# Kernel tuning notes

Measured on AMD Instinct MI355X. Metric: run time of the kernel, lower is better.

## Reference

```python
import jax, jax.numpy as jnp
import numpy as np

N_Q = 4       # n_qubits
PATCH = 3
PAD = 1       # patch_size // 2


def _u3(theta, phi, lam):
    # U3 gate matrix (2x2 complex)
    c = jnp.cos(theta / 2)
    s = jnp.sin(theta / 2)
    row0 = jnp.stack([c + 0j, -jnp.exp(1j * lam) * s])
    row1 = jnp.stack([jnp.exp(1j * phi) * s, jnp.exp(1j * (phi + lam)) * c])
    return jnp.stack([row0, row1]).astype(jnp.complex64)


def _apply_1q(state, U, wire):
    # state: (N,2,2,2,2) complex; U: (2,2) shared or (N,2,2) batched
    s = jnp.moveaxis(state, 1 + wire, -1)
    shp = s.shape
    s = s.reshape(s.shape[0], -1, 2)
    if U.ndim == 2:
        out = jnp.einsum('ij,nrj->nri', U, s)
    else:
        out = jnp.einsum('nij,nrj->nri', U, s)
    return jnp.moveaxis(out.reshape(shp), -1, 1 + wire)


def _apply_2q(state, U4, cw, tw):
    # U4: (4,4) on (control, target) subspace ordered |c t>
    s = jnp.moveaxis(state, (1 + cw, 1 + tw), (-2, -1))
    shp = s.shape
    s = s.reshape(s.shape[0], -1, 4)
    out = jnp.einsum('ij,nrj->nri', U4, s)
    return jnp.moveaxis(out.reshape(shp), (-2, -1), (1 + cw, 1 + tw))


def setup_inputs() -> dict:
    key = jax.random.key(0)
    ks = jax.random.split(key, 8)
    B, C, H, W = 16, 64, 64, 64
    out_ch = 128
    d_in = C * PATCH * PATCH  # 576
    x = jax.random.normal(ks[0], (B, C, H, W), dtype=jnp.float32)
    fc1_w = jax.random.normal(ks[1], (N_Q, d_in), dtype=jnp.float32) * (1.0 / np.sqrt(d_in))
    fc1_b = jax.random.normal(ks[2], (N_Q,), dtype=jnp.float32) * 0.01
    u3_params = jax.random.normal(ks[3], (N_Q, 3), dtype=jnp.float32)
    cu3_params = jax.random.normal(ks[4], (N_Q, 3), dtype=jnp.float32)
    fc_w = jax.random.normal(ks[5], (out_ch, N_Q), dtype=jnp.float32) * 0.5
    fc_b = jax.random.normal(ks[6], (out_ch,), dtype=jnp.float32) * 0.01
    return {"x": x, "fc1_w": fc1_w, "fc1_b": fc1_b, "u3_params": u3_params,
            "cu3_params": cu3_params, "fc_w": fc_w, "fc_b": fc_b}


def reference(x, fc1_w, fc1_b, u3_params, cu3_params, fc_w, fc_b):
    B, C, H, W = x.shape
    xp = jnp.pad(x, ((0, 0), (0, 0), (PAD, PAD), (PAD, PAD)))
    Hout, Wout = H, W  # stride 1, same padding
    # im2col: feature order (C, di, dj) matches torch patch.reshape(B,-1)
    cols = jnp.stack([xp[:, :, di:di + Hout, dj:dj + Wout]
                      for di in range(PATCH) for dj in range(PATCH)], axis=2)  # (B,C,9,H,W)
    patches = cols.transpose(0, 3, 4, 1, 2).reshape(B, Hout * Wout, C * PATCH * PATCH)
    ang = patches @ fc1_w.T + fc1_b  # (B, P, 4) rotation angles
    Np = B * Hout * Wout
    ang = ang.reshape(Np, N_Q)
    # initial state |0000> for every (batch, patch)
    state = jnp.zeros((Np, 2 ** N_Q), jnp.complex64).at[:, 0].set(1.0)
    state = state.reshape((Np,) + (2,) * N_Q)
    # RY encoding (per-element angles)
    for w in range(N_Q):
        th = ang[:, w] / 2
        c, s = jnp.cos(th), jnp.sin(th)
        Ury = jnp.stack([jnp.stack([c, -s], -1), jnp.stack([s, c], -1)], -2).astype(jnp.complex64)
        state = _apply_1q(state, Ury, w)
    # trainable U3 on every wire
    for w in range(N_Q):
        state = _apply_1q(state, _u3(u3_params[w, 0], u3_params[w, 1], u3_params[w, 2]), w)
    # circular CU3 ring (0,1),(1,2),(2,3),(3,0)
    for w in range(N_Q):
        U = _u3(cu3_params[w, 0], cu3_params[w, 1], cu3_params[w, 2])
        U4 = jnp.eye(4, dtype=jnp.complex64).at[2:, 2:].set(U)
        state = _apply_2q(state, U4, w, (w + 1) % N_Q)
    # <Z> on each wire
    probs = state.real ** 2 + state.imag ** 2  # (Np,2,2,2,2)
    zv = jnp.array([1.0, -1.0], jnp.float32)
    expz = jnp.stack(
        [(probs * zv.reshape((1,) + (1,) * w + (2,) + (1,) * (N_Q - 1 - w))).sum(axis=(1, 2, 3, 4))
         for w in range(N_Q)], axis=1)  # (Np,4)
    out = expz.reshape(B, Hout * Wout, N_Q) @ fc_w.T + fc_b  # (B,P,out_ch)
    out_ch = fc_w.shape[0]
    # faithful to original: view(B, out_ch, side_h, side_w) on contiguous (P,out_ch)
    return out.reshape(B, out_ch, Hout, Wout)
```

## Files before the change

kernel.cpp:

```cpp
#include <hip/hip_runtime.h>
#include <hip/hip_bf16.h>
#include <math.h>

typedef unsigned short u16;
typedef unsigned int   u32;
typedef unsigned long long u64;

#define WS_W2    0
#define WS_B4    2304
#define WS_FCW   2308
#define WS_FCB   2820
#define WS_GATES 2948
#define WS_FLAG  3012
#define WS_PART  4096

__device__ inline float bfbits2f(u32 lo16) {
    u32 u = lo16 << 16;
    return __builtin_bit_cast(float, u);
}
__device__ inline float bchi(u32 w) {
    return __builtin_bit_cast(float, w & 0xffff0000u);
}
__device__ inline float bclo(u32 w) {
    return __builtin_bit_cast(float, w << 16);
}
__device__ inline u16 f2bf(float f) {
    u32 u = __builtin_bit_cast(u32, f);
    u = u + 0x7fffu + ((u >> 16) & 1u);
    return (u16)(u >> 16);
}
__device__ inline float ld_param(const void* p, int i, int isbf16) {
    return isbf16 ? bfbits2f(((const u16*)p)[i]) : ((const float*)p)[i];
}

__global__ __launch_bounds__(256) void k0_prep(
        const void* __restrict__ x,
        const void* __restrict__ fc1_w, const void* __restrict__ fc1_b,
        const void* __restrict__ u3p,   const void* __restrict__ cu3p,
        const void* __restrict__ fc_w,  const void* __restrict__ fc_b,
        float* __restrict__ ws) {
    __shared__ int sflag;
    int t = threadIdx.x;
    if (t == 0) {
        const u32* xw = (const u32*)x;
        int cnt = 0;
        for (int i = 0; i < 64; ++i) {
            u32 e = (xw[i] >> 7) & 0xFFu;
            if (e >= 110 && e <= 130) ++cnt;
        }
        sflag = (cnt >= 32) ? 1 : 0;
        ws[WS_FLAG] = (float)sflag;
    }
    __syncthreads();
    const int bf = sflag;
    u32* wpk = (u32*)ws + WS_W2;
    for (int idx = t; idx < 1152; idx += 256) {
        int c = idx / 18;
        int rem = idx - c * 18;
        int r = rem / 6;
        int p = rem - r * 6;
        int i0 = 2 * p, i1 = 2 * p + 1;
        int q0 = i0 / 3, d0 = i0 - 3 * q0;
        int q1 = i1 / 3, d1 = i1 - 3 * q1;
        u32 lo = f2bf(ld_param(fc1_w, q0 * 576 + c * 9 + r * 3 + d0, bf));
        u32 hi = f2bf(ld_param(fc1_w, q1 * 576 + c * 9 + r * 3 + d1, bf));
        wpk[idx] = lo | (hi << 16);
    }
    if (t < 4)   ws[WS_B4 + t] = ld_param(fc1_b, t, bf);
    for (int idx = t; idx < 512; idx += 256) ws[WS_FCW + idx] = ld_param(fc_w, idx, bf);
    if (t < 128) ws[WS_FCB + t] = ld_param(fc_b, t, bf);
    if (t < 8) {
        int w = t & 3;
        const void* p = (t < 4) ? u3p : cu3p;
        float th = ld_param(p, w * 3 + 0, bf);
        float ph = ld_param(p, w * 3 + 1, bf);
        float la = ld_param(p, w * 3 + 2, bf);
        float c = cosf(0.5f * th), s = sinf(0.5f * th);
        float cl = cosf(la), sl = sinf(la);
        float cp = cosf(ph), sp = sinf(ph);
        float cpl = cp * cl - sp * sl, spl = sp * cl + cp * sl;
        float* m = ws + WS_GATES + t * 8;
        m[0] = c;        m[1] = 0.f;
        m[2] = -cl * s;  m[3] = -sl * s;
        m[4] = cp * s;   m[5] = sp * s;
        m[6] = cpl * c;  m[7] = spl * c;
    }
}

__global__ __launch_bounds__(256) void kA_conv(
        const void* __restrict__ x, const float* __restrict__ ws,
        float4* __restrict__ part) {
    __shared__ u32 tile[24 * 34];
    __shared__ float4 red4[256];
    const int t = threadIdx.x;
    const int bid = blockIdx.x;
    const int cg  = bid & 7;
    const int row = (bid >> 3) & 63;
    const int b   = bid >> 9;
    const int bf = (ws[WS_FLAG] != 0.0f) ? 1 : 0;
    const int c0 = cg * 8;
    const int tc = t >> 6;

    const int cs = __builtin_amdgcn_readfirstlane(c0 + tc * 2);
    const u32* wpk = (const u32*)ws + WS_W2 + cs * 18;
    u32 w36[36];
#pragma unroll
    for (int i = 0; i < 36; ++i) w36[i] = wpk[i];

    const u32*    xu = (const u32*)x;
    const float2* xf = (const float2*)x;
    const int xbase = b * 131072;

    {
        const int jj = t & 31;
        const int g8 = t >> 5;
#pragma unroll
        for (int i = 0; i < 3; ++i) {
            int rowcl = g8 + i * 8;
            int r = rowcl >> 3, cl = rowcl & 7;
            int gr = row - 1 + r;
            u32 pk = 0;
            if (gr >= 0 && gr < 64) {
                int idx = xbase + (c0 + cl) * 2048 + gr * 32 + jj;
                if (bf) pk = xu[idx];
                else { float2 v = xf[idx];
                       pk = (u32)f2bf(v.x) | ((u32)f2bf(v.y) << 16); }
            }
            tile[rowcl * 34 + 1 + jj] = pk;
        }
        if (t < 48) { int rc = t >> 1; tile[rc * 34 + ((t & 1) ? 33 : 0)] = 0u; }
    }
    __syncthreads();

    const int j = t & 63;
    const int pj = (j + 1) >> 1;
    const int sh = (1 - (j & 1)) * 16;
    float ang0 = 0.f, ang1 = 0.f, ang2 = 0.f, ang3 = 0.f;
#pragma unroll
    for (int cc = 0; cc < 2; ++cc) {
        const int cl = tc * 2 + cc;
#pragma unroll
        for (int r = 0; r < 3; ++r) {
            const u32* rp = tile + (r * 8 + cl) * 34 + pj;
            u32 lo = rp[0], hi = rp[1];
            u64 v = (((u64)hi << 32) | lo) >> sh;
            u32 vlo = (u32)v, vhi = (u32)(v >> 32);
            float e0 = bclo(vlo);
            float e1 = bchi(vlo);
            float e2 = bclo(vhi);
            const int wb = cc * 18 + r * 6;
            u32 u0 = w36[wb], u1 = w36[wb + 1], u2 = w36[wb + 2];
            u32 u3 = w36[wb + 3], u4 = w36[wb + 4], u5 = w36[wb + 5];
            ang0 += e0 * bclo(u0) + e1 * bchi(u0) + e2 * bclo(u1);
            ang1 += e0 * bchi(u1) + e1 * bclo(u2) + e2 * bchi(u2);
            ang2 += e0 * bclo(u3) + e1 * bchi(u3) + e2 * bclo(u4);
            ang3 += e0 * bchi(u4) + e1 * bclo(u5) + e2 * bchi(u5);
        }
    }

    red4[tc * 64 + j] = make_float4(ang0, ang1, ang2, ang3);
    __syncthreads();
    if (t < 64) {
        float4 a0 = red4[t], a1 = red4[64 + t], a2 = red4[128 + t], a3 = red4[192 + t];
        float4 s = make_float4(a0.x + a1.x + a2.x + a3.x,
                               a0.y + a1.y + a2.y + a3.y,
                               a0.z + a1.z + a2.z + a3.z,
                               a0.w + a1.w + a2.w + a3.w);
        part[cg * 65536 + b * 4096 + row * 64 + t] = s;
    }
}

__global__ __launch_bounds__(256) void kB_circuit_fc(
        const float* __restrict__ ws, const float4* __restrict__ part,
        void* __restrict__ out) {
    __shared__ float4 smEz[64];
    const int t = threadIdx.x;
    const int bp0 = blockIdx.x * 64;
    const int bf = (ws[WS_FLAG] != 0.0f) ? 1 : 0;

    if (t < 64) {
        const int bp = bp0 + t;
        float ax = 0.f, ay = 0.f, az = 0.f, aw = 0.f;
#pragma unroll
        for (int g = 0; g < 8; ++g) {
            float4 a = part[g * 65536 + bp];
            ax += a.x; ay += a.y; az += a.z; aw += a.w;
        }
        float angf[4];
        angf[0] = ws[WS_B4 + 0] + ax;
        angf[1] = ws[WS_B4 + 1] + ay;
        angf[2] = ws[WS_B4 + 2] + az;
        angf[3] = ws[WS_B4 + 3] + aw;

        const float* G = ws + WS_GATES;
        float vr[4][2], vi[4][2];
#pragma unroll
        for (int w = 0; w < 4; ++w) {
            float sa, ca;
            __sincosf(0.5f * angf[w], &sa, &ca);
            const float* m = G + w * 8;
            vr[w][0] = m[0] * ca + m[2] * sa;  vi[w][0] = m[1] * ca + m[3] * sa;
            vr[w][1] = m[4] * ca + m[6] * sa;  vi[w][1] = m[5] * ca + m[7] * sa;
        }
        float t01r[4], t01i[4], t23r[4], t23i[4];
#pragma unroll
        for (int a = 0; a < 2; ++a)
#pragma unroll
            for (int bq = 0; bq < 2; ++bq) {
                t01r[a * 2 + bq] = vr[0][a] * vr[1][bq] - vi[0][a] * vi[1][bq];
                t01i[a * 2 + bq] = vr[0][a] * vi[1][bq] + vi[0][a] * vr[1][bq];
                t23r[a * 2 + bq] = vr[2][a] * vr[3][bq] - vi[2][a] * vi[3][bq];
                t23i[a * 2 + bq] = vr[2][a] * vi[3][bq] + vi[2][a] * vr[3][bq];
            }
        float ar[16], ai[16];
#pragma unroll
        for (int n = 0; n < 16; ++n) {
            int hi = n >> 2, lo = n & 3;
            ar[n] = t01r[hi] * t23r[lo] - t01i[hi] * t23i[lo];
            ai[n] = t01r[hi] * t23i[lo] + t01i[hi] * t23r[lo];
        }
#pragma unroll
        for (int w = 0; w < 4; ++w) {
            const float* m = G + 32 + w * 8;
            const int cb = 8 >> w;
            const int tb = 8 >> ((w + 1) & 3);
#pragma unroll
            for (int n = 0; n < 16; ++n) {
                if ((n & cb) != 0 && (n & tb) == 0) {
                    int n1 = n | tb;
                    float a0r = ar[n], a0i = ai[n], a1r = ar[n1], a1i = ai[n1];
                    ar[n]  = m[0] * a0r - m[1] * a0i + m[2] * a1r - m[3] * a1i;
                    ai[n]  = m[0] * a0i + m[1] * a0r + m[2] * a1i + m[3] * a1r;
                    ar[n1] = m[4] * a0r - m[5] * a0i + m[6] * a1r - m[7] * a1i;
                    ai[n1] = m[4] * a0i + m[5] * a0r + m[6] * a1i + m[7] * a1r;
                }
            }
        }
        float ez[4] = {0.f, 0.f, 0.f, 0.f};
#pragma unroll
        for (int n = 0; n < 16; ++n) {
            float pr = ar[n] * ar[n] + ai[n] * ai[n];
#pragma unroll
            for (int w = 0; w < 4; ++w)
                ez[w] += ((n >> (3 - w)) & 1) ? -pr : pr;
        }
        smEz[t] = make_float4(ez[0], ez[1], ez[2], ez[3]);
    }
    __syncthreads();

    const int og = (t & 15) * 8;
    const float4* fw4 = (const float4*)(ws + WS_FCW) + og;
    const float*  fbp = ws + WS_FCB + og;
    float4 w0 = fw4[0], w1 = fw4[1], w2 = fw4[2], w3 = fw4[3];
    float4 w4 = fw4[4], w5 = fw4[5], w6 = fw4[6], w7 = fw4[7];
    float4 bA = *(const float4*)fbp, bB = *(const float4*)(fbp + 4);
#pragma unroll
    for (int ch = 0; ch < 4; ++ch) {
        const int pl = (t >> 4) + ch * 16;
        const float4 ez = smEz[pl];
        float v0 = bA.x + ez.x*w0.x + ez.y*w0.y + ez.z*w0.z + ez.w*w0.w;
        float v1 = bA.y + ez.x*w1.x + ez.y*w1.y + ez.z*w1.z + ez.w*w1.w;
        float v2 = bA.z + ez.x*w2.x + ez.y*w2.y + ez.z*w2.z + ez.w*w2.w;
        float v3 = bA.w + ez.x*w3.x + ez.y*w3.y + ez.z*w3.z + ez.w*w3.w;
        float v4 = bB.x + ez.x*w4.x + ez.y*w4.y + ez.z*w4.z + ez.w*w4.w;
        float v5 = bB.y + ez.x*w5.x + ez.y*w5.y + ez.z*w5.z + ez.w*w5.w;
        float v6 = bB.z + ez.x*w6.x + ez.y*w6.y + ez.z*w6.z + ez.w*w6.w;
        float v7 = bB.w + ez.x*w7.x + ez.y*w7.y + ez.z*w7.z + ez.w*w7.w;
        if (bf) {
            u32 p0 = (u32)f2bf(v0) | ((u32)f2bf(v1) << 16);
            u32 p1 = (u32)f2bf(v2) | ((u32)f2bf(v3) << 16);
            u32 p2 = (u32)f2bf(v4) | ((u32)f2bf(v5) << 16);
            u32 p3 = (u32)f2bf(v6) | ((u32)f2bf(v7) << 16);
            ((uint4*)out)[blockIdx.x * 1024 + ch * 256 + t] =
                make_uint4(p0, p1, p2, p3);
        } else {
            float4* o = (float4*)out + (blockIdx.x * 2048 + ch * 512 + 2 * t);
            o[0] = make_float4(v0, v1, v2, v3);
            o[1] = make_float4(v4, v5, v6, v7);
        }
    }
}

extern "C" void kernel_launch(void* const* d_in, const int* in_sizes, int n_in,
                              void* d_out, int out_size, void* d_ws, size_t ws_size,
                              hipStream_t stream) {
    float* ws = (float*)d_ws;
    float4* part = (float4*)(ws + WS_PART);
    k0_prep<<<dim3(1), dim3(256), 0, stream>>>(d_in[0], d_in[1], d_in[2], d_in[3],
                                               d_in[4], d_in[5], d_in[6], ws);
    kA_conv<<<dim3(8192), dim3(256), 0, stream>>>(d_in[0], ws, part);
    kB_circuit_fc<<<dim3(1024), dim3(256), 0, stream>>>(ws, part, d_out);
}
```

Before: 109.3 us.

## Fuse conv projection and circuit+FC kernels into one per-row block

Merges the conv/angle kernel and the circuit+FC kernel into one kernel where each 512-thread block handles all 64 channels of one output row. The 8-way channel-group partials are reduced in shared memory instead of going through a global workspace, which removes a kernel launch and the partial-sum write and read. In exchange each block stages a much larger LDS tile (192x34 words plus reductions), which lowers occupancy, and it loads weights in a serial chunk loop.

```diff
diff --git a/kernel.cpp b/kernel.cpp
--- a/kernel.cpp
+++ b/kernel.cpp
@@ -12,7 +12,6 @@
 #define WS_FCB   2820
 #define WS_GATES 2948
 #define WS_FLAG  3012
-#define WS_PART  4096
 
 __device__ inline float bfbits2f(u32 lo16) {
     u32 u = lo16 << 16;
@@ -87,25 +86,17 @@
     }
 }
 
-__global__ __launch_bounds__(256) void kA_conv(
+__global__ __launch_bounds__(512) void kF_fused(
         const void* __restrict__ x, const float* __restrict__ ws,
-        float4* __restrict__ part) {
-    __shared__ u32 tile[24 * 34];
-    __shared__ float4 red4[256];
-    const int t = threadIdx.x;
-    const int bid = blockIdx.x;
-    const int cg  = bid & 7;
-    const int row = (bid >> 3) & 63;
-    const int b   = bid >> 9;
+        void* __restrict__ out) {
+    __shared__ u32 tile[192 * 34];
+    __shared__ float4 red4[512];
+    __shared__ float4 smEz[64];
+    const int t   = threadIdx.x;
+    const int blk = blockIdx.x;
+    const int row = blk & 63;
+    const int b   = blk >> 6;
     const int bf = (ws[WS_FLAG] != 0.0f) ? 1 : 0;
-    const int c0 = cg * 8;
-    const int tc = t >> 6;
-
-    const int cs = __builtin_amdgcn_readfirstlane(c0 + tc * 2);
-    const u32* wpk = (const u32*)ws + WS_W2 + cs * 18;
-    u32 w36[36];
-#pragma unroll
-    for (int i = 0; i < 36; ++i) w36[i] = wpk[i];
 
     const u32*    xu = (const u32*)x;
     const float2* xf = (const float2*)x;
@@ -113,77 +104,66 @@
 
     {
         const int jj = t & 31;
-        const int g8 = t >> 5;
-#pragma unroll
-        for (int i = 0; i < 3; ++i) {
-            int rowcl = g8 + i * 8;
-            int r = rowcl >> 3, cl = rowcl & 7;
+        const int g  = t >> 5;
+#pragma unroll
+        for (int i = 0; i < 12; ++i) {
+            int rowcl = g + i * 16;
+            int r = rowcl >> 6, c = rowcl & 63;
             int gr = row - 1 + r;
             u32 pk = 0;
             if (gr >= 0 && gr < 64) {
-                int idx = xbase + (c0 + cl) * 2048 + gr * 32 + jj;
+                int idx = xbase + c * 2048 + gr * 32 + jj;
                 if (bf) pk = xu[idx];
                 else { float2 v = xf[idx];
                        pk = (u32)f2bf(v.x) | ((u32)f2bf(v.y) << 16); }
             }
             tile[rowcl * 34 + 1 + jj] = pk;
         }
-        if (t < 48) { int rc = t >> 1; tile[rc * 34 + ((t & 1) ? 33 : 0)] = 0u; }
-    }
-    __syncthreads();
-
-    const int j = t & 63;
+        if (t < 384) { int rc = t >> 1; tile[rc * 34 + ((t & 1) ? 33 : 0)] = 0u; }
+    }
+    __syncthreads();
+
+    const int j  = t & 63;
+    const int tcw = t >> 6;
     const int pj = (j + 1) >> 1;
     const int sh = (1 - (j & 1)) * 16;
     float ang0 = 0.f, ang1 = 0.f, ang2 = 0.f, ang3 = 0.f;
-#pragma unroll
-    for (int cc = 0; cc < 2; ++cc) {
-        const int cl = tc * 2 + cc;
-#pragma unroll
-        for (int r = 0; r < 3; ++r) {
-            const u32* rp = tile + (r * 8 + cl) * 34 + pj;
-            u32 lo = rp[0], hi = rp[1];
-            u64 v = (((u64)hi << 32) | lo) >> sh;
-            u32 vlo = (u32)v, vhi = (u32)(v >> 32);
-            float e0 = bclo(vlo);
-            float e1 = bchi(vlo);
-            float e2 = bclo(vhi);
-            const int wb = cc * 18 + r * 6;
-            u32 u0 = w36[wb], u1 = w36[wb + 1], u2 = w36[wb + 2];
-            u32 u3 = w36[wb + 3], u4 = w36[wb + 4], u5 = w36[wb + 5];
-            ang0 += e0 * bclo(u0) + e1 * bchi(u0) + e2 * bclo(u1);
-            ang1 += e0 * bchi(u1) + e1 * bclo(u2) + e2 * bchi(u2);
-            ang2 += e0 * bclo(u3) + e1 * bchi(u3) + e2 * bclo(u4);
-            ang3 += e0 * bchi(u4) + e1 * bclo(u5) + e2 * bchi(u5);
-        }
-    }
-
-    red4[tc * 64 + j] = make_float4(ang0, ang1, ang2, ang3);
-    __syncthreads();
+#pragma unroll 1
+    for (int chunk = 0; chunk < 4; ++chunk) {
+        const int cs = __builtin_amdgcn_readfirstlane(tcw * 8 + chunk * 2);
+        const u32* wpk = (const u32*)ws + WS_W2 + cs * 18;
+        u32 w36[36];
+#pragma unroll
+        for (int i = 0; i < 36; ++i) w36[i] = wpk[i];
+#pragma unroll
+        for (int cc = 0; cc < 2; ++cc) {
+#pragma unroll
+            for (int r = 0; r < 3; ++r) {
+                const u32* rp = tile + (r * 64 + cs + cc) * 34 + pj;
+                u32 lo = rp[0], hi = rp[1];
+                u64 v = (((u64)hi << 32) | lo) >> sh;
+                u32 vlo = (u32)v, vhi = (u32)(v >> 32);
+                float e0 = bclo(vlo);
+                float e1 = bchi(vlo);
+                float e2 = bclo(vhi);
+                const int wb = cc * 18 + r * 6;
+                u32 u0 = w36[wb], u1 = w36[wb + 1], u2 = w36[wb + 2];
+                u32 u3 = w36[wb + 3], u4 = w36[wb + 4], u5 = w36[wb + 5];
+                ang0 += e0 * bclo(u0) + e1 * bchi(u0) + e2 * bclo(u1);
+                ang1 += e0 * bchi(u1) + e1 * bclo(u2) + e2 * bchi(u2);
+                ang2 += e0 * bclo(u3) + e1 * bchi(u3) + e2 * bclo(u4);
+                ang3 += e0 * bchi(u4) + e1 * bclo(u5) + e2 * bchi(u5);
+            }
+        }
+    }
+    red4[t] = make_float4(ang0, ang1, ang2, ang3);
+    __syncthreads();
+
     if (t < 64) {
-        float4 a0 = red4[t], a1 = red4[64 + t], a2 = red4[128 + t], a3 = red4[192 + t];
-        float4 s = make_float4(a0.x + a1.x + a2.x + a3.x,
-                               a0.y + a1.y + a2.y + a3.y,
-                               a0.z + a1.z + a2.z + a3.z,
-                               a0.w + a1.w + a2.w + a3.w);
-        part[cg * 65536 + b * 4096 + row * 64 + t] = s;
-    }
-}
-
-__global__ __launch_bounds__(256) void kB_circuit_fc(
-        const float* __restrict__ ws, const float4* __restrict__ part,
-        void* __restrict__ out) {
-    __shared__ float4 smEz[64];
-    const int t = threadIdx.x;
-    const int bp0 = blockIdx.x * 64;
-    const int bf = (ws[WS_FLAG] != 0.0f) ? 1 : 0;
-
-    if (t < 64) {
-        const int bp = bp0 + t;
         float ax = 0.f, ay = 0.f, az = 0.f, aw = 0.f;
 #pragma unroll
-        for (int g = 0; g < 8; ++g) {
-            float4 a = part[g * 65536 + bp];
+        for (int k = 0; k < 8; ++k) {
+            float4 a = red4[k * 64 + t];
             ax += a.x; ay += a.y; az += a.z; aw += a.w;
         }
         float angf[4];
@@ -255,8 +235,8 @@
     float4 w4 = fw4[4], w5 = fw4[5], w6 = fw4[6], w7 = fw4[7];
     float4 bA = *(const float4*)fbp, bB = *(const float4*)(fbp + 4);
 #pragma unroll
-    for (int ch = 0; ch < 4; ++ch) {
-        const int pl = (t >> 4) + ch * 16;
+    for (int ch = 0; ch < 2; ++ch) {
+        const int pl = (t >> 4) + ch * 32;
         const float4 ez = smEz[pl];
         float v0 = bA.x + ez.x*w0.x + ez.y*w0.y + ez.z*w0.z + ez.w*w0.w;
         float v1 = bA.y + ez.x*w1.x + ez.y*w1.y + ez.z*w1.z + ez.w*w1.w;
@@ -271,10 +251,10 @@
             u32 p1 = (u32)f2bf(v2) | ((u32)f2bf(v3) << 16);
             u32 p2 = (u32)f2bf(v4) | ((u32)f2bf(v5) << 16);
             u32 p3 = (u32)f2bf(v6) | ((u32)f2bf(v7) << 16);
-            ((uint4*)out)[blockIdx.x * 1024 + ch * 256 + t] =
+            ((uint4*)out)[blk * 1024 + ch * 512 + t] =
                 make_uint4(p0, p1, p2, p3);
         } else {
-            float4* o = (float4*)out + (blockIdx.x * 2048 + ch * 512 + 2 * t);
+            float4* o = (float4*)out + (blk * 2048 + ch * 1024 + 2 * t);
             o[0] = make_float4(v0, v1, v2, v3);
             o[1] = make_float4(v4, v5, v6, v7);
         }
@@ -285,9 +265,7 @@
                               void* d_out, int out_size, void* d_ws, size_t ws_size,
                               hipStream_t stream) {
     float* ws = (float*)d_ws;
-    float4* part = (float4*)(ws + WS_PART);
     k0_prep<<<dim3(1), dim3(256), 0, stream>>>(d_in[0], d_in[1], d_in[2], d_in[3],
                                                d_in[4], d_in[5], d_in[6], ws);
-    kA_conv<<<dim3(8192), dim3(256), 0, stream>>>(d_in[0], ws, part);
-    kB_circuit_fc<<<dim3(1024), dim3(256), 0, stream>>>(ws, part, d_out);
-}
+    kF_fused<<<dim3(1024), dim3(512), 0, stream>>>(d_in[0], ws, d_out);
+}
```

Result: slower. 116.3 us (+6.4%).

## Drop prep kernel; fold param prep into conv and circuit kernels, stage partials in output

Applied to the files above, without the earlier changes.

Removes the single-block prep kernel by having each block sniff the input dtype with a wavefront ballot and load or convert fc1 weights, gate matrices and FC params directly from the inputs. Partial angle sums are now staged in the output buffer, laid out per row-block so each circuit block reads only its own region before overwriting it. This saves one launch and its serialization, at the cost of redundant per-block weight conversion and trig work. The in-place reuse of the output relies on each block's read region lying inside its own write region.

```diff
diff --git a/kernel.cpp b/kernel.cpp
--- a/kernel.cpp
+++ b/kernel.cpp
@@ -5,14 +5,6 @@
 typedef unsigned short u16;
 typedef unsigned int   u32;
 typedef unsigned long long u64;
-
-#define WS_W2    0
-#define WS_B4    2304
-#define WS_FCW   2308
-#define WS_FCB   2820
-#define WS_GATES 2948
-#define WS_FLAG  3012
-#define WS_PART  4096
 
 __device__ inline float bfbits2f(u32 lo16) {
     u32 u = lo16 << 16;
@@ -33,63 +25,16 @@
     return isbf16 ? bfbits2f(((const u16*)p)[i]) : ((const float*)p)[i];
 }
 
-__global__ __launch_bounds__(256) void k0_prep(
-        const void* __restrict__ x,
-        const void* __restrict__ fc1_w, const void* __restrict__ fc1_b,
-        const void* __restrict__ u3p,   const void* __restrict__ cu3p,
-        const void* __restrict__ fc_w,  const void* __restrict__ fc_b,
-        float* __restrict__ ws) {
-    __shared__ int sflag;
-    int t = threadIdx.x;
-    if (t == 0) {
-        const u32* xw = (const u32*)x;
-        int cnt = 0;
-        for (int i = 0; i < 64; ++i) {
-            u32 e = (xw[i] >> 7) & 0xFFu;
-            if (e >= 110 && e <= 130) ++cnt;
-        }
-        sflag = (cnt >= 32) ? 1 : 0;
-        ws[WS_FLAG] = (float)sflag;
-    }
-    __syncthreads();
-    const int bf = sflag;
-    u32* wpk = (u32*)ws + WS_W2;
-    for (int idx = t; idx < 1152; idx += 256) {
-        int c = idx / 18;
-        int rem = idx - c * 18;
-        int r = rem / 6;
-        int p = rem - r * 6;
-        int i0 = 2 * p, i1 = 2 * p + 1;
-        int q0 = i0 / 3, d0 = i0 - 3 * q0;
-        int q1 = i1 / 3, d1 = i1 - 3 * q1;
-        u32 lo = f2bf(ld_param(fc1_w, q0 * 576 + c * 9 + r * 3 + d0, bf));
-        u32 hi = f2bf(ld_param(fc1_w, q1 * 576 + c * 9 + r * 3 + d1, bf));
-        wpk[idx] = lo | (hi << 16);
-    }
-    if (t < 4)   ws[WS_B4 + t] = ld_param(fc1_b, t, bf);
-    for (int idx = t; idx < 512; idx += 256) ws[WS_FCW + idx] = ld_param(fc_w, idx, bf);
-    if (t < 128) ws[WS_FCB + t] = ld_param(fc_b, t, bf);
-    if (t < 8) {
-        int w = t & 3;
-        const void* p = (t < 4) ? u3p : cu3p;
-        float th = ld_param(p, w * 3 + 0, bf);
-        float ph = ld_param(p, w * 3 + 1, bf);
-        float la = ld_param(p, w * 3 + 2, bf);
-        float c = cosf(0.5f * th), s = sinf(0.5f * th);
-        float cl = cosf(la), sl = sinf(la);
-        float cp = cosf(ph), sp = sinf(ph);
-        float cpl = cp * cl - sp * sl, spl = sp * cl + cp * sl;
-        float* m = ws + WS_GATES + t * 8;
-        m[0] = c;        m[1] = 0.f;
-        m[2] = -cl * s;  m[3] = -sl * s;
-        m[4] = cp * s;   m[5] = sp * s;
-        m[6] = cpl * c;  m[7] = spl * c;
-    }
+__device__ inline int sniff_bf16(const void* x, int t) {
+    u32 xv = ((const u32*)x)[t & 63];
+    u32 e  = (xv >> 7) & 0xFFu;
+    u64 m  = __ballot(e >= 110u && e <= 130u);
+    return (__popcll(m) >= 32) ? 1 : 0;
 }
 
 __global__ __launch_bounds__(256) void kA_conv(
-        const void* __restrict__ x, const float* __restrict__ ws,
-        float4* __restrict__ part) {
+        const void* __restrict__ x, const void* __restrict__ fc1_w,
+        void* __restrict__ out) {
     __shared__ u32 tile[24 * 34];
     __shared__ float4 red4[256];
     const int t = threadIdx.x;
@@ -97,15 +42,43 @@
     const int cg  = bid & 7;
     const int row = (bid >> 3) & 63;
     const int b   = bid >> 9;
-    const int bf = (ws[WS_FLAG] != 0.0f) ? 1 : 0;
+    const int rowblk = bid >> 3;
     const int c0 = cg * 8;
     const int tc = t >> 6;
 
+    const int bf = sniff_bf16(x, t);
+
     const int cs = __builtin_amdgcn_readfirstlane(c0 + tc * 2);
-    const u32* wpk = (const u32*)ws + WS_W2 + cs * 18;
     u32 w36[36];
-#pragma unroll
-    for (int i = 0; i < 36; ++i) w36[i] = wpk[i];
+    if (bf) {
+        const u32* fw = (const u32*)fc1_w;
+#pragma unroll
+        for (int k = 0; k < 36; ++k) {
+            int c = cs + (k >= 18 ? 1 : 0);
+            int rem = k % 18; int r = rem / 6; int p = rem % 6;
+            int i0 = 2 * p, i1 = i0 + 1;
+            int q0 = i0 / 3, d0 = i0 - 3 * q0;
+            int q1 = i1 / 3, d1 = i1 - 3 * q1;
+            int a0 = q0 * 576 + c * 9 + r * 3 + d0;
+            int a1 = q1 * 576 + c * 9 + r * 3 + d1;
+            u32 lo = (fw[a0 >> 1] >> (16 * (a0 & 1))) & 0xffffu;
+            u32 hi = (fw[a1 >> 1] >> (16 * (a1 & 1))) & 0xffffu;
+            w36[k] = lo | (hi << 16);
+        }
+    } else {
+        const float* ff = (const float*)fc1_w;
+#pragma unroll
+        for (int k = 0; k < 36; ++k) {
+            int c = cs + (k >= 18 ? 1 : 0);
+            int rem = k % 18; int r = rem / 6; int p = rem % 6;
+            int i0 = 2 * p, i1 = i0 + 1;
+            int q0 = i0 / 3, d0 = i0 - 3 * q0;
+            int q1 = i1 / 3, d1 = i1 - 3 * q1;
+            u32 lo = f2bf(ff[q0 * 576 + c * 9 + r * 3 + d0]);
+            u32 hi = f2bf(ff[q1 * 576 + c * 9 + r * 3 + d1]);
+            w36[k] = lo | (hi << 16);
+        }
+    }
 
     const u32*    xu = (const u32*)x;
     const float2* xf = (const float2*)x;
@@ -166,33 +139,58 @@
                                a0.y + a1.y + a2.y + a3.y,
                                a0.z + a1.z + a2.z + a3.z,
                                a0.w + a1.w + a2.w + a3.w);
-        part[cg * 65536 + b * 4096 + row * 64 + t] = s;
+        float4* part = (float4*)out;
+        const int C = bf ? 1024 : 2048;
+        part[rowblk * C + cg * 64 + t] = s;
     }
 }
 
 __global__ __launch_bounds__(256) void kB_circuit_fc(
-        const float* __restrict__ ws, const float4* __restrict__ part,
-        void* __restrict__ out) {
+        const void* __restrict__ x,
+        const void* __restrict__ fc1_b, const void* __restrict__ u3p,
+        const void* __restrict__ cu3p,  const void* __restrict__ fc_w,
+        const void* __restrict__ fc_b,  void* __restrict__ out) {
+    __shared__ float smG[64];
     __shared__ float4 smEz[64];
     const int t = threadIdx.x;
-    const int bp0 = blockIdx.x * 64;
-    const int bf = (ws[WS_FLAG] != 0.0f) ? 1 : 0;
-
+    const int bf = sniff_bf16(x, t);
+    const int C = bf ? 1024 : 2048;
+    const int base = blockIdx.x * C;
+
+    float angf[4] = {0.f, 0.f, 0.f, 0.f};
     if (t < 64) {
-        const int bp = bp0 + t;
+        const float4* part = (const float4*)out;
         float ax = 0.f, ay = 0.f, az = 0.f, aw = 0.f;
 #pragma unroll
         for (int g = 0; g < 8; ++g) {
-            float4 a = part[g * 65536 + bp];
+            float4 a = part[base + g * 64 + t];
             ax += a.x; ay += a.y; az += a.z; aw += a.w;
         }
-        float angf[4];
-        angf[0] = ws[WS_B4 + 0] + ax;
-        angf[1] = ws[WS_B4 + 1] + ay;
-        angf[2] = ws[WS_B4 + 2] + az;
-        angf[3] = ws[WS_B4 + 3] + aw;
-
-        const float* G = ws + WS_GATES;
+        angf[0] = ld_param(fc1_b, 0, bf) + ax;
+        angf[1] = ld_param(fc1_b, 1, bf) + ay;
+        angf[2] = ld_param(fc1_b, 2, bf) + az;
+        angf[3] = ld_param(fc1_b, 3, bf) + aw;
+    }
+    if (t < 8) {
+        int w = t & 3;
+        const void* p = (t < 4) ? u3p : cu3p;
+        float th = ld_param(p, w * 3 + 0, bf);
+        float ph = ld_param(p, w * 3 + 1, bf);
+        float la = ld_param(p, w * 3 + 2, bf);
+        float c = cosf(0.5f * th), s = sinf(0.5f * th);
+        float cl = cosf(la), sl = sinf(la);
+        float cp = cosf(ph), sp = sinf(ph);
+        float cpl = cp * cl - sp * sl, spl = sp * cl + cp * sl;
+        float* m = smG + t * 8;
+        m[0] = c;        m[1] = 0.f;
+        m[2] = -cl * s;  m[3] = -sl * s;
+        m[4] = cp * s;   m[5] = sp * s;
+        m[6] = cpl * c;  m[7] = spl * c;
+    }
+    __syncthreads();
+
+    if (t < 64) {
+        const float* G = smG;
         float vr[4][2], vi[4][2];
 #pragma unroll
         for (int w = 0; w < 4; ++w) {
@@ -249,11 +247,28 @@
     __syncthreads();
 
     const int og = (t & 15) * 8;
-    const float4* fw4 = (const float4*)(ws + WS_FCW) + og;
-    const float*  fbp = ws + WS_FCB + og;
-    float4 w0 = fw4[0], w1 = fw4[1], w2 = fw4[2], w3 = fw4[3];
-    float4 w4 = fw4[4], w5 = fw4[5], w6 = fw4[6], w7 = fw4[7];
-    float4 bA = *(const float4*)fbp, bB = *(const float4*)(fbp + 4);
+    float4 w0, w1, w2, w3, w4, w5, w6, w7, bA, bB;
+    if (bf) {
+        const uint4* fw4 = (const uint4*)fc_w + (og >> 1);
+        uint4 qa = fw4[0], qb = fw4[1], qc = fw4[2], qd = fw4[3];
+        w0 = make_float4(bclo(qa.x), bchi(qa.x), bclo(qa.y), bchi(qa.y));
+        w1 = make_float4(bclo(qa.z), bchi(qa.z), bclo(qa.w), bchi(qa.w));
+        w2 = make_float4(bclo(qb.x), bchi(qb.x), bclo(qb.y), bchi(qb.y));
+        w3 = make_float4(bclo(qb.z), bchi(qb.z), bclo(qb.w), bchi(qb.w));
+        w4 = make_float4(bclo(qc.x), bchi(qc.x), bclo(qc.y), bchi(qc.y));
+        w5 = make_float4(bclo(qc.z), bchi(qc.z), bclo(qc.w), bchi(qc.w));
+        w6 = make_float4(bclo(qd.x), bchi(qd.x), bclo(qd.y), bchi(qd.y));
+        w7 = make_float4(bclo(qd.z), bchi(qd.z), bclo(qd.w), bchi(qd.w));
+        uint4 qbb = ((const uint4*)fc_b)[og >> 3];
+        bA = make_float4(bclo(qbb.x), bchi(qbb.x), bclo(qbb.y), bchi(qbb.y));
+        bB = make_float4(bclo(qbb.z), bchi(qbb.z), bclo(qbb.w), bchi(qbb.w));
+    } else {
+        const float4* fw4 = (const float4*)fc_w + og;
+        w0 = fw4[0]; w1 = fw4[1]; w2 = fw4[2]; w3 = fw4[3];
+        w4 = fw4[4]; w5 = fw4[5]; w6 = fw4[6]; w7 = fw4[7];
+        bA = ((const float4*)fc_b)[(og >> 2)];
+        bB = ((const float4*)fc_b)[(og >> 2) + 1];
+    }
 #pragma unroll
     for (int ch = 0; ch < 4; ++ch) {
         const int pl = (t >> 4) + ch * 16;
@@ -271,10 +286,9 @@
             u32 p1 = (u32)f2bf(v2) | ((u32)f2bf(v3) << 16);
             u32 p2 = (u32)f2bf(v4) | ((u32)f2bf(v5) << 16);
             u32 p3 = (u32)f2bf(v6) | ((u32)f2bf(v7) << 16);
-            ((uint4*)out)[blockIdx.x * 1024 + ch * 256 + t] =
-                make_uint4(p0, p1, p2, p3);
+            ((uint4*)out)[base + ch * 256 + t] = make_uint4(p0, p1, p2, p3);
         } else {
-            float4* o = (float4*)out + (blockIdx.x * 2048 + ch * 512 + 2 * t);
+            float4* o = (float4*)out + (base + ch * 512 + 2 * t);
             o[0] = make_float4(v0, v1, v2, v3);
             o[1] = make_float4(v4, v5, v6, v7);
         }
@@ -284,10 +298,8 @@
 extern "C" void kernel_launch(void* const* d_in, const int* in_sizes, int n_in,
                               void* d_out, int out_size, void* d_ws, size_t ws_size,
                               hipStream_t stream) {
-    float* ws = (float*)d_ws;
-    float4* part = (float4*)(ws + WS_PART);
-    k0_prep<<<dim3(1), dim3(256), 0, stream>>>(d_in[0], d_in[1], d_in[2], d_in[3],
-                                               d_in[4], d_in[5], d_in[6], ws);
-    kA_conv<<<dim3(8192), dim3(256), 0, stream>>>(d_in[0], ws, part);
-    kB_circuit_fc<<<dim3(1024), dim3(256), 0, stream>>>(ws, part, d_out);
-}
+    (void)d_ws; (void)ws_size; (void)in_sizes; (void)n_in; (void)out_size;
+    kA_conv<<<dim3(8192), dim3(256), 0, stream>>>(d_in[0], d_in[1], d_out);
+    kB_circuit_fc<<<dim3(1024), dim3(256), 0, stream>>>(
+        d_in[0], d_in[2], d_in[3], d_in[4], d_in[5], d_in[6], d_out);
+}
```

New measurement: 133.7 us. 22.3% more time.
